# Performance work log

Hardware: AMD Instinct MI355X
Metric: run time of the kernel (lower is better)

## Reference

```python
import jax, jax.numpy as jnp
import numpy as np

B, S, C = 64, 512, 512   # batch, subseq_length, in_features
H, D = 4, 128            # n_heads, hidden_features (H*D == C)
LN_EPS = 1e-5


def setup_inputs() -> dict:
    key = jax.random.key(0)
    k_h, k_w, k_b = jax.random.split(key, 3)
    h = jax.random.normal(k_h, (B, S, C), dtype=jnp.float32)
    # stacked per-head Linear weights, stored as [H, in, hid] for x @ W
    W = jax.random.normal(k_w, (H, C, D), dtype=jnp.float32) * (1.0 / np.sqrt(C))
    b = jax.random.normal(k_b, (H, D), dtype=jnp.float32) * 0.01
    adj = jnp.ones((S, S), dtype=jnp.float32)
    gamma = jnp.ones((C,), dtype=jnp.float32)
    beta = jnp.zeros((C,), dtype=jnp.float32)
    return {"t": 0, "h": h, "W": W, "b": b, "adj": adj, "gamma": gamma, "beta": beta}


def reference(t, h, W, b, adj, gamma, beta):
    # per-head projection: [H, B, S, D]
    hp = jnp.einsum("bsc,hcd->hbsd", h, W) + b[:, None, None, :]
    # raw scores, multiplicative adjacency mask (non-standard: mask BEFORE softmax by multiply)
    scores = jnp.einsum("hbsd,hbtd->hbst", hp, hp) * adj
    attn = jax.nn.softmax(scores, axis=-1)
    out = jnp.einsum("hbst,hbtd->hbsd", attn, hp)
    # concat heads along feature dim -> [B, S, H*D] == [B, S, C]
    out = jnp.transpose(out, (1, 2, 0, 3)).reshape(h.shape[0], h.shape[1], -1)
    # LayerNorm over last dim
    mu = jnp.mean(out, axis=-1, keepdims=True)
    var = jnp.mean(jnp.square(out - mu), axis=-1, keepdims=True)
    out = (out - mu) * jax.lax.rsqrt(var + LN_EPS) * gamma + beta
    # GELU (exact erf form, matching torch nn.GELU default)
    return jax.nn.gelu(out, approximate=False)
```

## Files before the change

### kernel.cpp

```cpp
#include <hip/hip_runtime.h>
#include <stdint.h>


typedef float  f32x4   __attribute__((ext_vector_type(4)));
typedef short  bf16x8  __attribute__((ext_vector_type(8)));
typedef unsigned short ushort8 __attribute__((ext_vector_type(8)));
typedef unsigned int   uint2v  __attribute__((ext_vector_type(2)));

#define GLD16(src, dst)                                                        \
  __builtin_amdgcn_global_load_lds(                                            \
      (const __attribute__((address_space(1))) void*)(src),                    \
      (__attribute__((address_space(3))) void*)(dst), 16, 0, 0)

__device__ __forceinline__ unsigned short f32_to_bf16(float x) {
  union { float f; unsigned int u; } v; v.f = x;
  unsigned int r = v.u + 0x7FFFu + ((v.u >> 16) & 1u);
  return (unsigned short)(r >> 16);
}
__device__ __forceinline__ float bf16_to_f32(unsigned int h) {
  union { float f; unsigned int u; } v; v.u = h << 16;
  return v.f;
}
__device__ __forceinline__ f32x4 mfma16(bf16x8 a, bf16x8 b, f32x4 c) {
  return __builtin_amdgcn_mfma_f32_16x16x32_bf16(a, b, c, 0, 0, 0);
}
__device__ __forceinline__ float bperm_f(int srcLane, float v) {
  return __int_as_float(__builtin_amdgcn_ds_bpermute(srcLane << 2, __float_as_int(v)));
}
__device__ __forceinline__ uint2v tr_read(const unsigned short* p) {
  uint2v r;
  asm volatile("ds_read_b64_tr_b16 %0, %1"
               : "=v"(r)
               : "v"((const __attribute__((address_space(3))) void*)p)
               : "memory");
  return r;
}

__global__ __launch_bounds__(256) void cast_split_h(
    const float* __restrict__ src, unsigned short* __restrict__ dhi,
    unsigned short* __restrict__ dlo) {
  size_t i = ((size_t)blockIdx.x * 256 + threadIdx.x) * 8;
  f32x4 a = *(const f32x4*)(src + i);
  f32x4 b = *(const f32x4*)(src + i + 4);
  ushort8 hi, lo;
#pragma unroll
  for (int e = 0; e < 4; ++e) {
    unsigned short h0 = f32_to_bf16(a[e]);
    hi[e] = h0; lo[e] = f32_to_bf16(a[e] - bf16_to_f32(h0));
    unsigned short h1 = f32_to_bf16(b[e]);
    hi[4 + e] = h1; lo[4 + e] = f32_to_bf16(b[e] - bf16_to_f32(h1));
  }
  *(ushort8*)(dhi + i) = hi;
  *(ushort8*)(dlo + i) = lo;
}

__global__ __launch_bounds__(256) void cast_split_Wt(
    const float* __restrict__ W, unsigned short* __restrict__ whi,
    unsigned short* __restrict__ wlo) {
  int o = blockIdx.x * 256 + threadIdx.x;
  int hd = o >> 16;
  int rem = o & 65535;
  int d = rem >> 9;
  int c = rem & 511;
  float v = W[((size_t)(hd * 512 + c)) * 128 + d];
  unsigned short h0 = f32_to_bf16(v);
  whi[o] = h0;
  wlo[o] = f32_to_bf16(v - bf16_to_f32(h0));
}

__global__ __launch_bounds__(256) void cast_adj(
    const float* __restrict__ src, unsigned short* __restrict__ dst) {
  size_t i = ((size_t)blockIdx.x * 256 + threadIdx.x) * 8;
  f32x4 a = *(const f32x4*)(src + i);
  f32x4 b = *(const f32x4*)(src + i + 4);
  ushort8 o;
#pragma unroll
  for (int e = 0; e < 4; ++e) {
    o[e] = f32_to_bf16(a[e]);
    o[4 + e] = f32_to_bf16(b[e]);
  }
  *(ushort8*)(dst + i) = o;
}

__global__ __launch_bounds__(256, 2) void proj_gemm(
    const unsigned short* __restrict__ ahi, const unsigned short* __restrict__ alo,
    const unsigned short* __restrict__ whi, const unsigned short* __restrict__ wlo,
    const float* __restrict__ bias, unsigned short* __restrict__ hp_hi,
    unsigned short* __restrict__ hp_lo) {
  int bid = blockIdx.x;
  int swz = (bid & 7) * 128 + (bid >> 3);
  int nt = swz & 3, mt = swz >> 2;
  int m0 = mt * 128, n0 = nt * 128;

  __shared__ alignas(16) unsigned short PSM[32768];

  int tid = threadIdx.x, wv = tid >> 6, lane = tid & 63;
  int l15 = lane & 15, l4 = lane >> 4;
  int wr = wv >> 1, wc = wv & 1;

  f32x4 acc[4][4];
#pragma unroll
  for (int a = 0; a < 4; ++a)
#pragma unroll
    for (int b = 0; b < 4; ++b) acc[a][b] = (f32x4){0.f, 0.f, 0.f, 0.f};

  for (int i = wv; i < 32; i += 4) {
    int grp = i >> 3, j = i & 7;
    int row = j * 16 + (lane >> 2);
    int off = (lane & 3) * 16;
    int sw = ((row >> 1) & 3) << 4;
    const unsigned short* sb = (grp == 0) ? ahi : (grp == 1) ? alo
                             : (grp == 2) ? whi : wlo;
    size_t srcoff = (grp < 2) ? ((size_t)(m0 + row) * 512) * 2
                              : ((size_t)(nt * 128 + row) * 512) * 2;
    GLD16((const char*)sb + srcoff + (off ^ sw), PSM + grp * 4096 + j * 512);
  }
  asm volatile("s_waitcnt vmcnt(0)" ::: "memory");
  __syncthreads();

  for (int ks = 0; ks < 16; ++ks) {
    const unsigned short* base = PSM + (ks & 1) * 16384;
    if (ks < 15) {
      unsigned short* nb = PSM + ((ks + 1) & 1) * 16384;
      int k1 = (ks + 1) * 32;
      for (int i = wv; i < 32; i += 4) {
        int grp = i >> 3, j = i & 7;
        int row = j * 16 + (lane >> 2);
        int off = (lane & 3) * 16;
        int sw = ((row >> 1) & 3) << 4;
        const unsigned short* sb = (grp == 0) ? ahi : (grp == 1) ? alo
                                 : (grp == 2) ? whi : wlo;
        size_t srcoff = (grp < 2) ? ((size_t)(m0 + row) * 512 + k1) * 2
                                  : ((size_t)(nt * 128 + row) * 512 + k1) * 2;
        GLD16((const char*)sb + srcoff + (off ^ sw), nb + grp * 4096 + j * 512);
      }
    }

    const unsigned short* Ah = base;
    const unsigned short* Al = base + 4096;
    const unsigned short* Bh = base + 8192;
    const unsigned short* Bl = base + 12288;
    bf16x8 fah[4], fal[4], fbh[4], fbl[4];
#pragma unroll
    for (int f = 0; f < 4; ++f) {
      int mr = wr * 64 + f * 16 + l15;
      int aadr = mr * 64 + ((16 * l4) ^ (((mr >> 1) & 3) << 4));
      fah[f] = *(const bf16x8*)((const char*)Ah + aadr);
      fal[f] = *(const bf16x8*)((const char*)Al + aadr);
      int nr = wc * 64 + f * 16 + l15;
      int badr = nr * 64 + ((16 * l4) ^ (((nr >> 1) & 3) << 4));
      fbh[f] = *(const bf16x8*)((const char*)Bh + badr);
      fbl[f] = *(const bf16x8*)((const char*)Bl + badr);
    }
#pragma unroll
    for (int a = 0; a < 4; ++a)
#pragma unroll
      for (int b = 0; b < 4; ++b) {
        acc[a][b] = mfma16(fah[a], fbh[b], acc[a][b]);
        acc[a][b] = mfma16(fah[a], fbl[b], acc[a][b]);
        acc[a][b] = mfma16(fal[a], fbh[b], acc[a][b]);
      }
    asm volatile("s_waitcnt vmcnt(0) lgkmcnt(0)" ::: "memory");
    __syncthreads();
  }

  unsigned short* Eh = PSM;
  unsigned short* El = PSM + 4096;
#pragma unroll
  for (int a = 0; a < 4; ++a) {
    __syncthreads();
#pragma unroll
    for (int b = 0; b < 4; ++b) {
      int cloc = wc * 64 + b * 16 + l15;
      float bv = bias[n0 + cloc];
#pragma unroll
      for (int r = 0; r < 4; ++r) {
        int rloc = wr * 16 + 4 * l4 + r;
        float v = acc[a][b][r] + bv;
        unsigned short hh = f32_to_bf16(v);
        Eh[rloc * 128 + cloc] = hh;
        El[rloc * 128 + cloc] = f32_to_bf16(v - bf16_to_f32(hh));
      }
    }
    __syncthreads();
    int rr = tid >> 3, c16 = (tid & 7) * 16;
    int mg = m0 + (rr >> 4) * 64 + a * 16 + (rr & 15);
    bf16x8 vh0 = *(const bf16x8*)(Eh + rr * 128 + c16);
    bf16x8 vh1 = *(const bf16x8*)(Eh + rr * 128 + c16 + 8);
    bf16x8 vl0 = *(const bf16x8*)(El + rr * 128 + c16);
    bf16x8 vl1 = *(const bf16x8*)(El + rr * 128 + c16 + 8);
    *(bf16x8*)(hp_hi + (size_t)mg * 512 + n0 + c16) = vh0;
    *(bf16x8*)(hp_hi + (size_t)mg * 512 + n0 + c16 + 8) = vh1;
    *(bf16x8*)(hp_lo + (size_t)mg * 512 + n0 + c16) = vl0;
    *(bf16x8*)(hp_lo + (size_t)mg * 512 + n0 + c16 + 8) = vl1;
  }
}

__global__ __launch_bounds__(256, 3) void attn_kernel(
    const unsigned short* __restrict__ hp_hi, const unsigned short* __restrict__ hp_lo,
    const unsigned short* __restrict__ adjb, unsigned short* __restrict__ ob) {
  int bid = blockIdx.x;
  int swz = (bid & 7) * 256 + (bid >> 3);
  int qt = swz & 7;
  int hd = (swz >> 3) & 3;
  int bb = swz >> 5;
  int q0 = qt * 64;

  __shared__ alignas(16) unsigned short SM[24576];

  int tid = threadIdx.x, w = tid >> 6, lane = tid & 63;
  int l15 = lane & 15, l4 = lane >> 4;
  int qg = q0 + w * 16 + l15;

  bf16x8 qh[4], ql[4];
  {
    size_t base = ((size_t)bb * 512 + qg) * 512 + hd * 128 + 8 * l4;
#pragma unroll
    for (int ds = 0; ds < 4; ++ds) {
      qh[ds] = *(const bf16x8*)(hp_hi + base + ds * 32);
      ql[ds] = *(const bf16x8*)(hp_lo + base + ds * 32);
    }
  }

  f32x4 o[8];
#pragma unroll
  for (int vf = 0; vf < 8; ++vf) o[vf] = (f32x4){0.f, 0.f, 0.f, 0.f};
  float m_run = -3.0e38f, l_run = 0.f;

  const unsigned short* ssb = (w & 2) ? hp_lo : hp_hi;
  int sdst = (w & 2) ? 4096 : 0;
  int sdbase = (w & 1) * 4;
  int skv = lane >> 1, sdh = lane & 1;

  {
    size_t rowb = ((size_t)(bb * 512 + skv)) * 1024 + hd * 256 + sdh * 16;
#pragma unroll
    for (int s2 = 0; s2 < 4; ++s2) {
      int sd = sdbase + s2;
      GLD16((const char*)ssb + rowb + sd * 32, SM + sdst + sd * 512);
    }
  }
  asm volatile("s_waitcnt vmcnt(0)" ::: "memory");
  __syncthreads();

  for (int t = 0; t < 16; ++t) {
    int kv0 = t * 32;
    const unsigned short* Kb = SM + ((t & 1) << 13);
    const unsigned short* Khi = Kb;
    const unsigned short* Klo = Kb + 4096;

    if (t < 15) {
      unsigned short* Nb = SM + (((t + 1) & 1) << 13) + sdst;
      size_t rowb = ((size_t)(bb * 512 + kv0 + 32 + skv)) * 1024 + hd * 256 + sdh * 16;
#pragma unroll
      for (int s2 = 0; s2 < 4; ++s2) {
        int sd = sdbase + s2;
        GLD16((const char*)ssb + rowb + sd * 32, Nb + sd * 512);
      }
    }
    uint2 ua0 = *(const uint2*)(adjb + (size_t)qg * 512 + kv0 + 4 * l4);
    uint2 ua1 = *(const uint2*)(adjb + (size_t)qg * 512 + kv0 + 16 + 4 * l4);
    f32x4 av0, av1;
    av0[0] = bf16_to_f32(ua0.x & 0xFFFFu); av0[1] = bf16_to_f32(ua0.x >> 16);
    av0[2] = bf16_to_f32(ua0.y & 0xFFFFu); av0[3] = bf16_to_f32(ua0.y >> 16);
    av1[0] = bf16_to_f32(ua1.x & 0xFFFFu); av1[1] = bf16_to_f32(ua1.x >> 16);
    av1[2] = bf16_to_f32(ua1.y & 0xFFFFu); av1[3] = bf16_to_f32(ua1.y >> 16);

    f32x4 sc0 = {0.f, 0.f, 0.f, 0.f}, sc1 = {0.f, 0.f, 0.f, 0.f};
#pragma unroll
    for (int ds = 0; ds < 4; ++ds) {
      int boff = (2 * ds + (l4 >> 1)) * 1024 + 16 * (l4 & 1);
      int a0 = boff + l15 * 32;
      int a1 = boff + (16 + l15) * 32;
      bf16x8 kh0 = *(const bf16x8*)((const char*)Khi + a0);
      bf16x8 kl0 = *(const bf16x8*)((const char*)Klo + a0);
      bf16x8 kh1 = *(const bf16x8*)((const char*)Khi + a1);
      bf16x8 kl1 = *(const bf16x8*)((const char*)Klo + a1);
      sc0 = mfma16(kh0, qh[ds], sc0); sc1 = mfma16(kh1, qh[ds], sc1);
      sc0 = mfma16(kh0, ql[ds], sc0); sc1 = mfma16(kh1, ql[ds], sc1);
      sc0 = mfma16(kl0, qh[ds], sc0); sc1 = mfma16(kl1, qh[ds], sc1);
    }

    float p0[4], p1[4];
    float tm = -3.0e38f;
#pragma unroll
    for (int r = 0; r < 4; ++r) {
      p0[r] = sc0[r] * av0[r];
      p1[r] = sc1[r] * av1[r];
      tm = fmaxf(tm, fmaxf(p0[r], p1[r]));
    }
    tm = fmaxf(tm, __shfl_xor(tm, 16));
    tm = fmaxf(tm, __shfl_xor(tm, 32));
    if (__any(tm > m_run + 8.0f)) {
      float mn = fmaxf(m_run, tm);
      float scl = __expf(m_run - mn);
      m_run = mn;
      l_run *= scl;
      f32x4 s4;
#pragma unroll
      for (int r = 0; r < 4; ++r) s4[r] = bperm_f(4 * l4 + r, scl);
#pragma unroll
      for (int vf = 0; vf < 8; ++vf)
#pragma unroll
        for (int r = 0; r < 4; ++r) o[vf][r] *= s4[r];
    }
    float ps = 0.f;
#pragma unroll
    for (int r = 0; r < 4; ++r) {
      p0[r] = __expf(p0[r] - m_run); ps += p0[r];
      p1[r] = __expf(p1[r] - m_run); ps += p1[r];
    }
    ps += __shfl_xor(ps, 16);
    ps += __shfl_xor(ps, 32);
    l_run += ps;

    union PU { bf16x8 v; unsigned u[4]; } pah;
#pragma unroll
    for (int i = 0; i < 4; ++i) {
      float fa = (i < 2) ? p0[2 * i] : p1[2 * (i - 2)];
      float fb = (i < 2) ? p0[2 * i + 1] : p1[2 * (i - 2) + 1];
      pah.u[i] = (__float_as_uint(fa) >> 16) |
                 (__float_as_uint(fb) & 0xFFFF0000u);
    }

    const unsigned short* trb = Khi + lane * 4;
    union VU { bf16x8 v; uint2v u2[2]; } vh[8];
#pragma unroll
    for (int vf = 0; vf < 8; ++vf) {
      vh[vf].u2[0] = tr_read(trb + vf * 512);
      vh[vf].u2[1] = tr_read(trb + vf * 512 + 256);
    }
    asm volatile("s_waitcnt lgkmcnt(0)" ::: "memory");
    __builtin_amdgcn_sched_barrier(0);
#pragma unroll
    for (int vf = 0; vf < 8; ++vf)
      o[vf] = mfma16(pah.v, vh[vf].v, o[vf]);
    asm volatile("s_waitcnt vmcnt(0) lgkmcnt(0)" ::: "memory");
    __syncthreads();
  }

  float rinv = 1.0f / l_run;
  f32x4 r4;
#pragma unroll
  for (int r = 0; r < 4; ++r) r4[r] = bperm_f(4 * l4 + r, rinv);
  float* wbase = (float*)SM + w * 2048;
#pragma unroll
  for (int vf = 0; vf < 8; ++vf)
#pragma unroll
    for (int r = 0; r < 4; ++r)
      wbase[(4 * l4 + r) * 128 + vf * 16 + l15] = o[vf][r] * r4[r];
  __syncthreads();
#pragma unroll
  for (int p = 0; p < 4; ++p) {
    int row = p * 4 + l4;
    f32x4 v0 = *(const f32x4*)(wbase + row * 128 + l15 * 8);
    f32x4 v1 = *(const f32x4*)(wbase + row * 128 + l15 * 8 + 4);
    ushort8 o8;
#pragma unroll
    for (int e = 0; e < 4; ++e) {
      o8[e] = f32_to_bf16(v0[e]);
      o8[4 + e] = f32_to_bf16(v1[e]);
    }
    size_t mg = (size_t)bb * 512 + q0 + w * 16 + row;
    *(ushort8*)(ob + mg * 512 + hd * 128 + l15 * 8) = o8;
  }
}

__global__ __launch_bounds__(256) void ln_gelu_kernel(
    const unsigned short* __restrict__ in, float* __restrict__ outp,
    const float* __restrict__ gamma, const float* __restrict__ beta) {
  int w = threadIdx.x >> 6, lane = threadIdx.x & 63;
  size_t row = (size_t)blockIdx.x * 4 + w;
  ushort8 v = *(const ushort8*)(in + row * 512 + lane * 8);
  float x[8];
#pragma unroll
  for (int e = 0; e < 8; ++e) x[e] = bf16_to_f32((unsigned int)(unsigned short)v[e]);
  float s = 0.f;
#pragma unroll
  for (int e = 0; e < 8; ++e) s += x[e];
#pragma unroll
  for (int off = 32; off >= 1; off >>= 1) s += __shfl_xor(s, off);
  float mu = s * (1.0f / 512.0f);
  float vs = 0.f;
#pragma unroll
  for (int e = 0; e < 8; ++e) {
    float d = x[e] - mu; vs += d * d;
  }
#pragma unroll
  for (int off = 32; off >= 1; off >>= 1) vs += __shfl_xor(vs, off);
  float rs = rsqrtf(vs * (1.0f / 512.0f) + 1e-5f);
  f32x4 g0 = *(const f32x4*)(gamma + lane * 8);
  f32x4 g1 = *(const f32x4*)(gamma + lane * 8 + 4);
  f32x4 b0 = *(const f32x4*)(beta + lane * 8);
  f32x4 b1 = *(const f32x4*)(beta + lane * 8 + 4);
  f32x4 y0, y1;
#pragma unroll
  for (int e = 0; e < 4; ++e) {
    float y = (x[e] - mu) * rs * g0[e] + b0[e];
    y0[e] = 0.5f * y * (1.0f + erff(y * 0.70710678118654752f));
    float z = (x[4 + e] - mu) * rs * g1[e] + b1[e];
    y1[e] = 0.5f * z * (1.0f + erff(z * 0.70710678118654752f));
  }
  float* p = outp + row * 512 + lane * 8;
  *(f32x4*)p = y0;
  *(f32x4*)(p + 4) = y1;
}

extern "C" void kernel_launch(void* const* d_in, const int* in_sizes, int n_in,
                              void* d_out, int out_size, void* d_ws, size_t ws_size,
                              hipStream_t stream) {
  const float* h     = (const float*)d_in[1];
  const float* W     = (const float*)d_in[2];
  const float* bias  = (const float*)d_in[3];
  const float* adj   = (const float*)d_in[4];
  const float* gamma = (const float*)d_in[5];
  const float* beta  = (const float*)d_in[6];
  float* out = (float*)d_out;

  unsigned short* ws = (unsigned short*)d_ws;
  unsigned short* h_hi   = ws;
  unsigned short* h_lo   = ws + 16777216;
  unsigned short* hp_hi  = ws + 33554432;
  unsigned short* hp_lo  = ws + 50331648;
  unsigned short* Wt_hi  = ws + 67108864;
  unsigned short* Wt_lo  = ws + 67371008;
  unsigned short* adj_bf = ws;
  unsigned short* ob     = ws + 16777216;

  cast_split_h<<<8192, 256, 0, stream>>>(h, h_hi, h_lo);
  cast_split_Wt<<<1024, 256, 0, stream>>>(W, Wt_hi, Wt_lo);
  proj_gemm<<<1024, 256, 0, stream>>>(h_hi, h_lo, Wt_hi, Wt_lo, bias, hp_hi, hp_lo);
  cast_adj<<<128, 256, 0, stream>>>(adj, adj_bf);
  attn_kernel<<<2048, 256, 0, stream>>>(hp_hi, hp_lo, adj_bf, ob);
  ln_gelu_kernel<<<8192, 256, 0, stream>>>(ob, out, gamma, beta);
}
```

Measured before the change: 216.0 us.

## Fuse fp32-to-bf16 hi/lo split of h into projection GEMM tile load

Removes the separate cast_split_h kernel and has proj_gemm read fp32 h directly, splitting it into truncated bf16 hi/lo parts in registers before writing to LDS. This drops a full write and read pass of the 64 MB split buffers. The GEMM loses its double-buffered async prefetch and becomes single-buffered with synchronous loads, which may expose memory latency. The hi part now uses truncation instead of round-to-nearest, with the lo residual making up the difference.

```diff
diff --git a/kernel.cpp b/kernel.cpp
--- a/kernel.cpp
+++ b/kernel.cpp
@@ -34,24 +34,6 @@
                : "v"((const __attribute__((address_space(3))) void*)p)
                : "memory");
   return r;
-}
-
-__global__ __launch_bounds__(256) void cast_split_h(
-    const float* __restrict__ src, unsigned short* __restrict__ dhi,
-    unsigned short* __restrict__ dlo) {
-  size_t i = ((size_t)blockIdx.x * 256 + threadIdx.x) * 8;
-  f32x4 a = *(const f32x4*)(src + i);
-  f32x4 b = *(const f32x4*)(src + i + 4);
-  ushort8 hi, lo;
-#pragma unroll
-  for (int e = 0; e < 4; ++e) {
-    unsigned short h0 = f32_to_bf16(a[e]);
-    hi[e] = h0; lo[e] = f32_to_bf16(a[e] - bf16_to_f32(h0));
-    unsigned short h1 = f32_to_bf16(b[e]);
-    hi[4 + e] = h1; lo[4 + e] = f32_to_bf16(b[e] - bf16_to_f32(h1));
-  }
-  *(ushort8*)(dhi + i) = hi;
-  *(ushort8*)(dlo + i) = lo;
 }
 
 __global__ __launch_bounds__(256) void cast_split_Wt(
@@ -83,7 +65,7 @@
 }
 
 __global__ __launch_bounds__(256, 2) void proj_gemm(
-    const unsigned short* __restrict__ ahi, const unsigned short* __restrict__ alo,
+    const float* __restrict__ hsrc,
     const unsigned short* __restrict__ whi, const unsigned short* __restrict__ wlo,
     const float* __restrict__ bias, unsigned short* __restrict__ hp_hi,
     unsigned short* __restrict__ hp_lo) {
@@ -92,11 +74,13 @@
   int nt = swz & 3, mt = swz >> 2;
   int m0 = mt * 128, n0 = nt * 128;
 
-  __shared__ alignas(16) unsigned short PSM[32768];
+  __shared__ alignas(16) unsigned short Ah[4096], Al[4096], Bh[4096], Bl[4096];
 
   int tid = threadIdx.x, wv = tid >> 6, lane = tid & 63;
   int l15 = lane & 15, l4 = lane >> 4;
   int wr = wv >> 1, wc = wv & 1;
+  int arow = tid >> 3;
+  int acol = (tid & 7) * 4;
 
   f32x4 acc[4][4];
 #pragma unroll
@@ -104,42 +88,39 @@
 #pragma unroll
     for (int b = 0; b < 4; ++b) acc[a][b] = (f32x4){0.f, 0.f, 0.f, 0.f};
 
-  for (int i = wv; i < 32; i += 4) {
-    int grp = i >> 3, j = i & 7;
-    int row = j * 16 + (lane >> 2);
-    int off = (lane & 3) * 16;
-    int sw = ((row >> 1) & 3) << 4;
-    const unsigned short* sb = (grp == 0) ? ahi : (grp == 1) ? alo
-                             : (grp == 2) ? whi : wlo;
-    size_t srcoff = (grp < 2) ? ((size_t)(m0 + row) * 512) * 2
-                              : ((size_t)(nt * 128 + row) * 512) * 2;
-    GLD16((const char*)sb + srcoff + (off ^ sw), PSM + grp * 4096 + j * 512);
-  }
-  asm volatile("s_waitcnt vmcnt(0)" ::: "memory");
-  __syncthreads();
-
   for (int ks = 0; ks < 16; ++ks) {
-    const unsigned short* base = PSM + (ks & 1) * 16384;
-    if (ks < 15) {
-      unsigned short* nb = PSM + ((ks + 1) & 1) * 16384;
-      int k1 = (ks + 1) * 32;
-      for (int i = wv; i < 32; i += 4) {
-        int grp = i >> 3, j = i & 7;
-        int row = j * 16 + (lane >> 2);
-        int off = (lane & 3) * 16;
-        int sw = ((row >> 1) & 3) << 4;
-        const unsigned short* sb = (grp == 0) ? ahi : (grp == 1) ? alo
-                                 : (grp == 2) ? whi : wlo;
-        size_t srcoff = (grp < 2) ? ((size_t)(m0 + row) * 512 + k1) * 2
-                                  : ((size_t)(nt * 128 + row) * 512 + k1) * 2;
-        GLD16((const char*)sb + srcoff + (off ^ sw), nb + grp * 4096 + j * 512);
-      }
-    }
-
-    const unsigned short* Ah = base;
-    const unsigned short* Al = base + 4096;
-    const unsigned short* Bh = base + 8192;
-    const unsigned short* Bl = base + 12288;
+    int k0 = ks * 32;
+    for (int i = wv; i < 16; i += 4) {
+      int grp = i >> 3, j = i & 7;
+      int row = j * 16 + (lane >> 2);
+      int off = (lane & 3) * 16;
+      int sw = ((row >> 1) & 3) << 4;
+      const unsigned short* sb = grp ? wlo : whi;
+      unsigned short* db = grp ? Bl : Bh;
+      GLD16((const char*)sb + ((size_t)(nt * 128 + row) * 512 + k0) * 2 + (off ^ sw),
+            db + j * 512);
+    }
+#pragma unroll
+    for (int j = 0; j < 4; ++j) {
+      int r = j * 32 + arow;
+      f32x4 x = *(const f32x4*)(hsrc + (size_t)(m0 + r) * 512 + k0 + acol);
+      unsigned ua = __float_as_uint(x[0]), ub = __float_as_uint(x[1]);
+      unsigned uc = __float_as_uint(x[2]), ud = __float_as_uint(x[3]);
+      uint2 ph, pl;
+      ph.x = (ua >> 16) | (ub & 0xFFFF0000u);
+      ph.y = (uc >> 16) | (ud & 0xFFFF0000u);
+      float ra = x[0] - __uint_as_float(ua & 0xFFFF0000u);
+      float rb = x[1] - __uint_as_float(ub & 0xFFFF0000u);
+      float rc = x[2] - __uint_as_float(uc & 0xFFFF0000u);
+      float rd = x[3] - __uint_as_float(ud & 0xFFFF0000u);
+      pl.x = (__float_as_uint(ra) >> 16) | (__float_as_uint(rb) & 0xFFFF0000u);
+      pl.y = (__float_as_uint(rc) >> 16) | (__float_as_uint(rd) & 0xFFFF0000u);
+      int boff = r * 64 + ((acol * 2) ^ (((r >> 1) & 3) << 4));
+      *(uint2*)((char*)Ah + boff) = ph;
+      *(uint2*)((char*)Al + boff) = pl;
+    }
+    __syncthreads();
+
     bf16x8 fah[4], fal[4], fbh[4], fbl[4];
 #pragma unroll
     for (int f = 0; f < 4; ++f) {
@@ -160,12 +141,9 @@
         acc[a][b] = mfma16(fah[a], fbl[b], acc[a][b]);
         acc[a][b] = mfma16(fal[a], fbh[b], acc[a][b]);
       }
-    asm volatile("s_waitcnt vmcnt(0) lgkmcnt(0)" ::: "memory");
     __syncthreads();
   }
 
-  unsigned short* Eh = PSM;
-  unsigned short* El = PSM + 4096;
 #pragma unroll
   for (int a = 0; a < 4; ++a) {
     __syncthreads();
@@ -178,17 +156,17 @@
         int rloc = wr * 16 + 4 * l4 + r;
         float v = acc[a][b][r] + bv;
         unsigned short hh = f32_to_bf16(v);
-        Eh[rloc * 128 + cloc] = hh;
-        El[rloc * 128 + cloc] = f32_to_bf16(v - bf16_to_f32(hh));
+        Ah[rloc * 128 + cloc] = hh;
+        Al[rloc * 128 + cloc] = f32_to_bf16(v - bf16_to_f32(hh));
       }
     }
     __syncthreads();
     int rr = tid >> 3, c16 = (tid & 7) * 16;
     int mg = m0 + (rr >> 4) * 64 + a * 16 + (rr & 15);
-    bf16x8 vh0 = *(const bf16x8*)(Eh + rr * 128 + c16);
-    bf16x8 vh1 = *(const bf16x8*)(Eh + rr * 128 + c16 + 8);
-    bf16x8 vl0 = *(const bf16x8*)(El + rr * 128 + c16);
-    bf16x8 vl1 = *(const bf16x8*)(El + rr * 128 + c16 + 8);
+    bf16x8 vh0 = *(const bf16x8*)(Ah + rr * 128 + c16);
+    bf16x8 vh1 = *(const bf16x8*)(Ah + rr * 128 + c16 + 8);
+    bf16x8 vl0 = *(const bf16x8*)(Al + rr * 128 + c16);
+    bf16x8 vl1 = *(const bf16x8*)(Al + rr * 128 + c16 + 8);
     *(bf16x8*)(hp_hi + (size_t)mg * 512 + n0 + c16) = vh0;
     *(bf16x8*)(hp_hi + (size_t)mg * 512 + n0 + c16 + 8) = vh1;
     *(bf16x8*)(hp_lo + (size_t)mg * 512 + n0 + c16) = vl0;
@@ -418,19 +396,16 @@
   float* out = (float*)d_out;
 
   unsigned short* ws = (unsigned short*)d_ws;
-  unsigned short* h_hi   = ws;
-  unsigned short* h_lo   = ws + 16777216;
+  unsigned short* adj_bf = ws;
+  unsigned short* ob     = ws + 16777216;
   unsigned short* hp_hi  = ws + 33554432;
   unsigned short* hp_lo  = ws + 50331648;
   unsigned short* Wt_hi  = ws + 67108864;
   unsigned short* Wt_lo  = ws + 67371008;
-  unsigned short* adj_bf = ws;
-  unsigned short* ob     = ws + 16777216;
-
-  cast_split_h<<<8192, 256, 0, stream>>>(h, h_hi, h_lo);
+
   cast_split_Wt<<<1024, 256, 0, stream>>>(W, Wt_hi, Wt_lo);
-  proj_gemm<<<1024, 256, 0, stream>>>(h_hi, h_lo, Wt_hi, Wt_lo, bias, hp_hi, hp_lo);
   cast_adj<<<128, 256, 0, stream>>>(adj, adj_bf);
+  proj_gemm<<<1024, 256, 0, stream>>>(h, Wt_hi, Wt_lo, bias, hp_hi, hp_lo);
   attn_kernel<<<2048, 256, 0, stream>>>(hp_hi, hp_lo, adj_bf, ob);
   ln_gelu_kernel<<<8192, 256, 0, stream>>>(ob, out, gamma, beta);
 }
```

Result: faster. 194.0 us (-10.2%).
